# Performance work log

Measured on AMD Instinct MI355X. Metric: run time of the kernel, lower is better.

Reference implementation:

```python
import jax, jax.numpy as jnp
import numpy as np

BLOCK = 256          # block_size
K_IN = 64            # in_features // block_size
K_OUT = 64           # out_features // block_size
K_HALF = BLOCK // 2 + 1  # 129
INIT_SCALE = 0.1


def setup_inputs() -> dict:
    key = jax.random.key(0)
    kx, kr, ki = jax.random.split(key, 3)
    x = jax.random.normal(kx, (2048, K_IN * BLOCK), dtype=jnp.float32)
    W_real = jax.random.normal(kr, (K_OUT, K_IN, K_HALF), dtype=jnp.float32) * INIT_SCALE
    W_imag = jax.random.normal(ki, (K_OUT, K_IN, K_HALF), dtype=jnp.float32) * INIT_SCALE
    # match __init__: DC and Nyquist bins have zero imaginary part
    W_imag = W_imag.at[..., 0].set(0.0)
    W_imag = W_imag.at[..., -1].set(0.0)
    return {"x": x, "W_real": W_real, "W_imag": W_imag}


def _full_spectrum(W_real, W_imag):
    # Reconstruct full conjugate-symmetric spectrum per block: (k_out,k_in,BLOCK)
    H = (W_real + 1j * W_imag).astype(jnp.complex64)          # half spectrum (...,K_HALF)
    nyq = H[..., -1:].real.astype(jnp.complex64)              # real Nyquist bin (even BLOCK)
    return jnp.concatenate(
        [H[..., :-1], nyq, jnp.conj(H[..., 1:-1])[..., ::-1]], axis=-1
    )


def reference(x, W_real, W_imag):
    B = x.shape[0]
    x_blocks = x.reshape(B, K_IN, BLOCK)                      # (B, k_in, b)
    X_fft = jnp.fft.fft(x_blocks, axis=-1)                    # (B, k_in, b) complex64
    W_full = _full_spectrum(W_real, W_imag)                   # (k_out, k_in, b)
    # block-circulant matvec in frequency domain, accumulated over input blocks
    out_fft = jnp.einsum('bjf,ijf->bif', X_fft, jnp.conj(W_full))
    out = jnp.fft.ifft(out_fft, axis=-1).real                 # (B, k_out, b)
    return out.reshape(B, K_OUT * BLOCK).astype(x.dtype)
```

## Files before the change

kernel.cpp:

```cpp
#include <hip/hip_runtime.h>

#define BATCH 2048
#define KIN   64
#define KOUT  64
#define NPT   256
#define NF    129
#define FSTRIDE (BATCH * KIN)
#define XPLANE ((size_t)NF * FSTRIDE)
#define WPLANE (NF * KIN * KOUT)
#define NFP 133

#define WAVE_SYNC() __asm__ volatile("s_waitcnt lgkmcnt(0)" ::: "memory")

__device__ __forceinline__ int PHI(int i) { return i + (i >> 5); }

template<int SIGN>
__device__ __forceinline__ void fft256_r4(float2* A, float2* B, int lane) {
  float2* src = A;
  float2* dst = B;
  const float C = SIGN * (6.28318530717958647692f / 256.f);
#pragma unroll
  for (int st = 0; st < 4; ++st) {
    const int m  = 1 << (2 * st);
    const int t  = lane;
    const int jm = t & ~(m - 1);
    float2 s0 = src[PHI(t)];
    float2 s1 = src[PHI(t + 64)];
    float2 s2 = src[PHI(t + 128)];
    float2 s3 = src[PHI(t + 192)];
    float sw, cw;
    __sincosf(C * (float)jm, &sw, &cw);
    float c2 = cw * cw - sw * sw, s2w = 2.f * cw * sw;
    float c3 = c2 * cw - s2w * sw, s3w = c2 * sw + s2w * cw;
    float apcx = s0.x + s2.x, apcy = s0.y + s2.y;
    float amcx = s0.x - s2.x, amcy = s0.y - s2.y;
    float bpdx = s1.x + s3.x, bpdy = s1.y + s3.y;
    float bmdx = s1.x - s3.x, bmdy = s1.y - s3.y;
    float sbx = (SIGN < 0) ? bmdy : -bmdy;
    float sby = (SIGN < 0) ? -bmdx : bmdx;
    float t1x = amcx + sbx, t1y = amcy + sby;
    float t3x = amcx - sbx, t3y = amcy - sby;
    float t2x = apcx - bpdx, t2y = apcy - bpdy;
    const int base = t + 3 * jm;
    dst[PHI(base)]         = make_float2(apcx + bpdx, apcy + bpdy);
    dst[PHI(base + m)]     = make_float2(cw * t1x - sw * t1y, cw * t1y + sw * t1x);
    dst[PHI(base + 2 * m)] = make_float2(c2 * t2x - s2w * t2y, c2 * t2y + s2w * t2x);
    dst[PHI(base + 3 * m)] = make_float2(c3 * t3x - s3w * t3y, c3 * t3y + s3w * t3x);
    WAVE_SYNC();
    float2* tmp = src; src = dst; dst = tmp;
  }
}

__global__ __launch_bounds__(256) void k0_wtrans(const float* __restrict__ Wre,
                                                 const float* __restrict__ Wim,
                                                 float* __restrict__ Wtr,
                                                 float* __restrict__ Wti) {
  __shared__ float T[32][33];
  const int f0 = blockIdx.y * 32;
  const int d0 = blockIdx.x * 32;
  const int t  = threadIdx.x;
  const int a  = t & 31, g = t >> 5;
#pragma unroll
  for (int pl = 0; pl < 2; ++pl) {
    const float* src = pl ? Wim : Wre;
    float* dst = pl ? Wti : Wtr;
    if (pl) __syncthreads();
#pragma unroll
    for (int it = 0; it < 4; ++it) {
      int dl = g + it * 8;
      int d  = d0 + dl;
      int s  = (d & 63) * 64 + (d >> 6);
      int f  = f0 + a;
      if (f < NF) T[dl][a] = src[(size_t)s * NF + f];
    }
    __syncthreads();
#pragma unroll
    for (int it = 0; it < 4; ++it) {
      int fl = g + it * 8;
      int f  = f0 + fl;
      if (f < NF) dst[(size_t)f * (KIN * KOUT) + d0 + a] = T[a][fl];
    }
  }
}

__global__ __launch_bounds__(256) void k1_rfft(const float* __restrict__ x,
                                               float* __restrict__ Xtr,
                                               float* __restrict__ Xti) {
  __shared__ float2 fbuf[4][2][264];
  __shared__ float Sr[32 * NFP];
  __shared__ float Si[32 * NFP];
  const int wave = threadIdx.x >> 6, lane = threadIdx.x & 63;
  const int b = blockIdx.x >> 1, h = blockIdx.x & 1;
  float2* A  = fbuf[wave][0];
  float2* Bp = fbuf[wave][1];
#pragma unroll
  for (int rr = 0; rr < 8; ++rr) {
    const int jt  = rr * 4 + wave;
    const int idx = b * 64 + h * 32 + jt;
    float4 v = reinterpret_cast<const float4*>(x + (size_t)idx * NPT)[lane];
    A[PHI(4 * lane + 0)] = make_float2(v.x, 0.f);
    A[PHI(4 * lane + 1)] = make_float2(v.y, 0.f);
    A[PHI(4 * lane + 2)] = make_float2(v.z, 0.f);
    A[PHI(4 * lane + 3)] = make_float2(v.w, 0.f);
    WAVE_SYNC();
    fft256_r4<-1>(A, Bp, lane);
    float2 z0 = A[PHI(lane)];
    float2 z1 = A[PHI(lane + 64)];
    Sr[jt * NFP + lane]      = z0.x;  Si[jt * NFP + lane]      = z0.y;
    Sr[jt * NFP + lane + 64] = z1.x;  Si[jt * NFP + lane + 64] = z1.y;
    if (lane == 0) {
      float2 z2 = A[PHI(128)];
      Sr[jt * NFP + 128] = z2.x;  Si[jt * NFP + 128] = z2.y;
    }
    WAVE_SYNC();
  }
  __syncthreads();
  const int c = threadIdx.x & 31;
  const size_t baseidx = (size_t)b * 64 + h * 32 + c;
#pragma unroll
  for (int it = 0; it < 17; ++it) {
    int f = (threadIdx.x >> 5) + it * 8;
    if (f < NF) {
      Xtr[(size_t)f * FSTRIDE + baseidx] = Sr[c * NFP + f];
      Xti[(size_t)f * FSTRIDE + baseidx] = Si[c * NFP + f];
    }
  }
}

__global__ __launch_bounds__(256) void k2_cgemm(float* __restrict__ Xr,
                                                float* __restrict__ Xi,
                                                const float* __restrict__ Wtr,
                                                const float* __restrict__ Wti) {
  __shared__ __align__(16) float Xlr[64 * 68];
  __shared__ __align__(16) float Xli[64 * 68];
  __shared__ __align__(16) float Wlr[64 * 68];
  __shared__ __align__(16) float Wli[64 * 68];

  const int f  = blockIdx.y;
  const int b0 = blockIdx.x * 64;
  const int t  = threadIdx.x;
  const size_t xbase = (size_t)f * FSTRIDE + (size_t)b0 * 64;
  const float* wpr = Wtr + (size_t)f * (KIN * KOUT);
  const float* wpi = Wti + (size_t)f * (KIN * KOUT);

#pragma unroll
  for (int it = 0; it < 4; ++it) {
    int n4 = (it * 256 + t) * 4;
    int j = n4 >> 6, i0 = n4 & 63;
    float4 wr = *reinterpret_cast<const float4*>(wpr + n4);
    float4 wi = *reinterpret_cast<const float4*>(wpi + n4);
    *reinterpret_cast<float4*>(&Wlr[j * 68 + i0]) = wr;
    *reinterpret_cast<float4*>(&Wli[j * 68 + i0]) = wi;
  }
#pragma unroll
  for (int it = 0; it < 4; ++it) {
    int n4 = (it * 256 + t) * 4;
    int r = n4 >> 6, j0 = n4 & 63;
    float4 xr = *reinterpret_cast<const float4*>(Xr + xbase + n4);
    float4 xi = *reinterpret_cast<const float4*>(Xi + xbase + n4);
    Xlr[(j0 + 0) * 68 + r] = xr.x; Xlr[(j0 + 1) * 68 + r] = xr.y;
    Xlr[(j0 + 2) * 68 + r] = xr.z; Xlr[(j0 + 3) * 68 + r] = xr.w;
    Xli[(j0 + 0) * 68 + r] = xi.x; Xli[(j0 + 1) * 68 + r] = xi.y;
    Xli[(j0 + 2) * 68 + r] = xi.z; Xli[(j0 + 3) * 68 + r] = xi.w;
  }
  __syncthreads();

  const int tx = t & 15, ty = t >> 4;
  const int i0 = tx * 4, r0 = ty * 4;
  float aR[4][4] = {};
  float aI[4][4] = {};

#pragma unroll 4
  for (int j = 0; j < 64; ++j) {
    float4 xr = *reinterpret_cast<const float4*>(&Xlr[j * 68 + r0]);
    float4 xi = *reinterpret_cast<const float4*>(&Xli[j * 68 + r0]);
    float4 wr = *reinterpret_cast<const float4*>(&Wlr[j * 68 + i0]);
    float4 wi = *reinterpret_cast<const float4*>(&Wli[j * 68 + i0]);
    float xra[4] = {xr.x, xr.y, xr.z, xr.w};
    float xia[4] = {xi.x, xi.y, xi.z, xi.w};
    float wra[4] = {wr.x, wr.y, wr.z, wr.w};
    float wia[4] = {wi.x, wi.y, wi.z, wi.w};
#pragma unroll
    for (int a = 0; a < 4; ++a)
#pragma unroll
      for (int c = 0; c < 4; ++c) {
        aR[a][c] += xra[a] * wra[c] + xia[a] * wia[c];
        aI[a][c] += xia[a] * wra[c] - xra[a] * wia[c];
      }
  }

#pragma unroll
  for (int a = 0; a < 4; ++a) {
    size_t g = xbase + (size_t)(r0 + a) * 64 + i0;
    *reinterpret_cast<float4*>(&Xr[g]) = make_float4(aR[a][0], aR[a][1], aR[a][2], aR[a][3]);
    *reinterpret_cast<float4*>(&Xi[g]) = make_float4(aI[a][0], aI[a][1], aI[a][2], aI[a][3]);
  }
}

__global__ __launch_bounds__(256) void k3_irfft(const float* __restrict__ Or,
                                                const float* __restrict__ Oi,
                                                float* __restrict__ out) {
  __shared__ float2 fbuf[4][2][264];
  __shared__ float Sr[32 * NFP];
  __shared__ float Si[32 * NFP];
  const int wave = threadIdx.x >> 6, lane = threadIdx.x & 63;
  const int b = blockIdx.x >> 1, h = blockIdx.x & 1;
  const int c = threadIdx.x & 31;
  const size_t baseidx = (size_t)b * 64 + h * 32 + c;
#pragma unroll
  for (int it = 0; it < 17; ++it) {
    int f = (threadIdx.x >> 5) + it * 8;
    if (f < NF) {
      Sr[c * NFP + f] = Or[(size_t)f * FSTRIDE + baseidx];
      Si[c * NFP + f] = Oi[(size_t)f * FSTRIDE + baseidx];
    }
  }
  __syncthreads();
  float2* A  = fbuf[wave][0];
  float2* Bp = fbuf[wave][1];
#pragma unroll
  for (int rr = 0; rr < 8; ++rr) {
    const int it8 = rr * 4 + wave;
    float re0 = Sr[it8 * NFP + lane],      im0 = Si[it8 * NFP + lane];
    float re1 = Sr[it8 * NFP + lane + 64], im1 = Si[it8 * NFP + lane + 64];
    A[PHI(lane)]      = make_float2(re0, im0);
    A[PHI(lane + 64)] = make_float2(re1, im1);
    if (lane) A[PHI(256 - lane)] = make_float2(re0, -im0);
    A[PHI(192 - lane)] = make_float2(re1, -im1);
    if (lane == 0)
      A[PHI(128)] = make_float2(Sr[it8 * NFP + 128], Si[it8 * NFP + 128]);
    WAVE_SYNC();
    fft256_r4<1>(A, Bp, lane);
    const float s = 1.0f / 256.f;
    float4 o;
    o.x = A[PHI(4 * lane + 0)].x * s;
    o.y = A[PHI(4 * lane + 1)].x * s;
    o.z = A[PHI(4 * lane + 2)].x * s;
    o.w = A[PHI(4 * lane + 3)].x * s;
    const int idx = b * 64 + h * 32 + it8;
    reinterpret_cast<float4*>(out + (size_t)idx * NPT)[lane] = o;
    WAVE_SYNC();
  }
}

extern "C" void kernel_launch(void* const* d_in, const int* in_sizes, int n_in,
                              void* d_out, int out_size, void* d_ws, size_t ws_size,
                              hipStream_t stream) {
  const float* x   = (const float*)d_in[0];
  const float* Wre = (const float*)d_in[1];
  const float* Wim = (const float*)d_in[2];
  float* out = (float*)d_out;
  float* ws  = (float*)d_ws;

  float* Xr  = ws;
  float* Xi  = ws + XPLANE;
  float* Wtr = ws + 2 * XPLANE;
  float* Wti = Wtr + WPLANE;

  hipLaunchKernelGGL(k0_wtrans, dim3(128, 5), dim3(256), 0, stream,
                     Wre, Wim, Wtr, Wti);
  hipLaunchKernelGGL(k1_rfft, dim3(BATCH * 2), dim3(256), 0, stream,
                     x, Xr, Xi);
  hipLaunchKernelGGL(k2_cgemm, dim3(BATCH / 64, NF), dim3(256), 0, stream,
                     Xr, Xi, Wtr, Wti);
  hipLaunchKernelGGL(k3_irfft, dim3(BATCH * 2), dim3(256), 0, stream,
                     Xr, Xi, out);
}
```

Measured before the change: 459.0 us.

## Pack two real FFTs per complex FFT, in-place swizzled radix-4, interleaved complex workspace

Replaces the ping-pong radix-4 FFT with in-place DIF/DIT stages over an XOR-swizzled shared buffer, with twiddles computed once per thread. Two real rows are packed into one complex 256-point FFT, so the forward and inverse transforms run half as many FFTs. The intermediate spectrum is stored as interleaved float2 instead of separate real and imaginary planes. The GEMM uses a swizzled X tile, and global loads are prefetched a step ahead. This cuts FFT arithmetic, LDS traffic and memory transactions, at the cost of more index math and register pressure.

```diff
diff --git a/kernel.cpp b/kernel.cpp
--- a/kernel.cpp
+++ b/kernel.cpp
@@ -12,43 +12,69 @@
 
 #define WAVE_SYNC() __asm__ volatile("s_waitcnt lgkmcnt(0)" ::: "memory")
 
-__device__ __forceinline__ int PHI(int i) { return i + (i >> 5); }
-
-template<int SIGN>
-__device__ __forceinline__ void fft256_r4(float2* A, float2* B, int lane) {
-  float2* src = A;
-  float2* dst = B;
-  const float C = SIGN * (6.28318530717958647692f / 256.f);
-#pragma unroll
-  for (int st = 0; st < 4; ++st) {
-    const int m  = 1 << (2 * st);
-    const int t  = lane;
-    const int jm = t & ~(m - 1);
-    float2 s0 = src[PHI(t)];
-    float2 s1 = src[PHI(t + 64)];
-    float2 s2 = src[PHI(t + 128)];
-    float2 s3 = src[PHI(t + 192)];
-    float sw, cw;
-    __sincosf(C * (float)jm, &sw, &cw);
-    float c2 = cw * cw - sw * sw, s2w = 2.f * cw * sw;
-    float c3 = c2 * cw - s2w * sw, s3w = c2 * sw + s2w * cw;
-    float apcx = s0.x + s2.x, apcy = s0.y + s2.y;
-    float amcx = s0.x - s2.x, amcy = s0.y - s2.y;
-    float bpdx = s1.x + s3.x, bpdy = s1.y + s3.y;
-    float bmdx = s1.x - s3.x, bmdy = s1.y - s3.y;
-    float sbx = (SIGN < 0) ? bmdy : -bmdy;
-    float sby = (SIGN < 0) ? -bmdx : bmdx;
-    float t1x = amcx + sbx, t1y = amcy + sby;
-    float t3x = amcx - sbx, t3y = amcy - sby;
-    float t2x = apcx - bpdx, t2y = apcy - bpdy;
-    const int base = t + 3 * jm;
-    dst[PHI(base)]         = make_float2(apcx + bpdx, apcy + bpdy);
-    dst[PHI(base + m)]     = make_float2(cw * t1x - sw * t1y, cw * t1y + sw * t1x);
-    dst[PHI(base + 2 * m)] = make_float2(c2 * t2x - s2w * t2y, c2 * t2y + s2w * t2x);
-    dst[PHI(base + 3 * m)] = make_float2(c3 * t3x - s3w * t3y, c3 * t3y + s3w * t3x);
-    WAVE_SYNC();
-    float2* tmp = src; src = dst; dst = tmp;
-  }
+__device__ __forceinline__ int SWZ(int i) {
+  return i ^ (((i >> 6) & 3) << 2) ^ ((i >> 4) & 3);
+}
+__device__ __forceinline__ int REV4(int f) {
+  return ((f & 3) << 6) | ((f & 12) << 2) | ((f >> 2) & 12) | ((f >> 6) & 3);
+}
+__device__ __forceinline__ float2 cmul(float2 v, float c, float s) {
+  return make_float2(v.x * c - v.y * s, v.y * c + v.x * s);
+}
+
+struct TW { float c1, s1, c2, s2, c3, s3; };
+__device__ __forceinline__ TW mk_tw(int unit, float C) {
+  TW t; float s, c;
+  __sincosf(C * (float)unit, &s, &c);
+  t.c1 = c; t.s1 = s;
+  t.c2 = c * c - s * s;  t.s2 = 2.f * c * s;
+  t.c3 = t.c2 * c - t.s2 * s;  t.s3 = t.c2 * s + t.s2 * c;
+  return t;
+}
+
+struct Quad { int i0, i1, i2, i3; };
+__device__ __forceinline__ Quad mkquad(int base, int M) {
+  Quad q;
+  q.i0 = SWZ(base); q.i1 = SWZ(base + M);
+  q.i2 = SWZ(base + 2 * M); q.i3 = SWZ(base + 3 * M);
+  return q;
+}
+
+template<bool TWID>
+__device__ __forceinline__ void dif_stage(float2* A, const Quad& q, const TW& w) {
+  float2 a0 = A[q.i0], a1 = A[q.i1], a2 = A[q.i2], a3 = A[q.i3];
+  float t0x = a0.x + a2.x, t0y = a0.y + a2.y;
+  float t1x = a0.x - a2.x, t1y = a0.y - a2.y;
+  float t2x = a1.x + a3.x, t2y = a1.y + a3.y;
+  float t3x = a1.x - a3.x, t3y = a1.y - a3.y;
+  float2 b0 = make_float2(t0x + t2x, t0y + t2y);
+  float2 b2 = make_float2(t0x - t2x, t0y - t2y);
+  float2 b1 = make_float2(t1x + t3y, t1y - t3x);
+  float2 b3 = make_float2(t1x - t3y, t1y + t3x);
+  A[q.i0] = b0;
+  A[q.i1] = TWID ? cmul(b1, w.c1, w.s1) : b1;
+  A[q.i2] = TWID ? cmul(b2, w.c2, w.s2) : b2;
+  A[q.i3] = TWID ? cmul(b3, w.c3, w.s3) : b3;
+  WAVE_SYNC();
+}
+
+template<bool TWID>
+__device__ __forceinline__ void dit_stage(float2* A, const Quad& q, const TW& w) {
+  float2 a0 = A[q.i0], a1 = A[q.i1], a2 = A[q.i2], a3 = A[q.i3];
+  if (TWID) {
+    a1 = cmul(a1, w.c1, w.s1);
+    a2 = cmul(a2, w.c2, w.s2);
+    a3 = cmul(a3, w.c3, w.s3);
+  }
+  float Ax = a0.x + a2.x, Ay = a0.y + a2.y;
+  float Bx = a0.x - a2.x, By = a0.y - a2.y;
+  float Cx = a1.x + a3.x, Cy = a1.y + a3.y;
+  float Dx = a1.x - a3.x, Dy = a1.y - a3.y;
+  A[q.i0] = make_float2(Ax + Cx, Ay + Cy);
+  A[q.i2] = make_float2(Ax - Cx, Ay - Cy);
+  A[q.i1] = make_float2(Bx - Dy, By + Dx);
+  A[q.i3] = make_float2(Bx + Dy, By - Dx);
+  WAVE_SYNC();
 }
 
 __global__ __launch_bounds__(256) void k0_wtrans(const float* __restrict__ Wre,
@@ -84,55 +110,99 @@
 }
 
 __global__ __launch_bounds__(256) void k1_rfft(const float* __restrict__ x,
-                                               float* __restrict__ Xtr,
-                                               float* __restrict__ Xti) {
-  __shared__ float2 fbuf[4][2][264];
-  __shared__ float Sr[32 * NFP];
-  __shared__ float Si[32 * NFP];
+                                               float2* __restrict__ Xc) {
+  __shared__ float2 fbuf[4][256];
+  __shared__ float Sr[16 * NFP];
+  __shared__ float Si[16 * NFP];
   const int wave = threadIdx.x >> 6, lane = threadIdx.x & 63;
   const int b = blockIdx.x >> 1, h = blockIdx.x & 1;
-  float2* A  = fbuf[wave][0];
-  float2* Bp = fbuf[wave][1];
-#pragma unroll
-  for (int rr = 0; rr < 8; ++rr) {
-    const int jt  = rr * 4 + wave;
-    const int idx = b * 64 + h * 32 + jt;
-    float4 v = reinterpret_cast<const float4*>(x + (size_t)idx * NPT)[lane];
-    A[PHI(4 * lane + 0)] = make_float2(v.x, 0.f);
-    A[PHI(4 * lane + 1)] = make_float2(v.y, 0.f);
-    A[PHI(4 * lane + 2)] = make_float2(v.z, 0.f);
-    A[PHI(4 * lane + 3)] = make_float2(v.w, 0.f);
-    WAVE_SYNC();
-    fft256_r4<-1>(A, Bp, lane);
-    float2 z0 = A[PHI(lane)];
-    float2 z1 = A[PHI(lane + 64)];
-    Sr[jt * NFP + lane]      = z0.x;  Si[jt * NFP + lane]      = z0.y;
-    Sr[jt * NFP + lane + 64] = z1.x;  Si[jt * NFP + lane + 64] = z1.y;
-    if (lane == 0) {
-      float2 z2 = A[PHI(128)];
-      Sr[jt * NFP + 128] = z2.x;  Si[jt * NFP + 128] = z2.y;
-    }
-    WAVE_SYNC();
-  }
-  __syncthreads();
-  const int c = threadIdx.x & 31;
-  const size_t baseidx = (size_t)b * 64 + h * 32 + c;
-#pragma unroll
-  for (int it = 0; it < 17; ++it) {
-    int f = (threadIdx.x >> 5) + it * 8;
-    if (f < NF) {
-      Xtr[(size_t)f * FSTRIDE + baseidx] = Sr[c * NFP + f];
-      Xti[(size_t)f * FSTRIDE + baseidx] = Si[c * NFP + f];
-    }
-  }
-}
-
-__global__ __launch_bounds__(256) void k2_cgemm(float* __restrict__ Xr,
-                                                float* __restrict__ Xi,
+  float2* A = fbuf[wave];
+
+  const Quad q0 = mkquad(lane, 64);
+  const Quad q1 = mkquad(((lane >> 4) << 6) + (lane & 15), 16);
+  const Quad q2 = mkquad(((lane >> 2) << 4) + (lane & 3), 4);
+  const Quad q3 = mkquad(lane << 2, 1);
+  const float C = -6.28318530717958647692f / 256.f;
+  const TW tw0 = mk_tw(lane, C);
+  const TW tw1 = mk_tw(4 * (lane & 15), C);
+  const TW tw2 = mk_tw(16 * (lane & 3), C);
+  const int uf  = SWZ(REV4(lane));
+  const int ug  = SWZ(REV4(lane + 64));
+  const int ufm = SWZ(REV4((256 - lane) & 255));
+  const int ugm = SWZ(REV4(192 - lane));
+
+  const size_t rowbase = (size_t)b * 64 + h * 32;
+  float4 va = reinterpret_cast<const float4*>(x + (rowbase + 2 * wave) * NPT)[lane];
+  float4 vb = reinterpret_cast<const float4*>(x + (rowbase + 2 * wave + 1) * NPT)[lane];
+
+#pragma unroll
+  for (int half = 0; half < 2; ++half) {
+    if (half) __syncthreads();
+#pragma unroll
+    for (int uu = 0; uu < 2; ++uu) {
+      const int u = half * 2 + uu;
+      const int p = u * 4 + wave;
+      float4 na = va, nb = vb;
+      if (u < 3) {
+        const size_t nidx = rowbase + 2 * ((u + 1) * 4 + wave);
+        na = reinterpret_cast<const float4*>(x + nidx * NPT)[lane];
+        nb = reinterpret_cast<const float4*>(x + (nidx + 1) * NPT)[lane];
+      }
+      A[q3.i0] = make_float2(va.x, vb.x);
+      A[q3.i1] = make_float2(va.y, vb.y);
+      A[q3.i2] = make_float2(va.z, vb.z);
+      A[q3.i3] = make_float2(va.w, vb.w);
+      WAVE_SYNC();
+      dif_stage<true >(A, q0, tw0);
+      dif_stage<true >(A, q1, tw1);
+      dif_stage<true >(A, q2, tw2);
+      dif_stage<false>(A, q3, tw0);
+      float2 zf  = A[uf];
+      float2 zg  = A[ug];
+      float2 zfm = A[ufm];
+      float2 zgm = A[ugm];
+      const int r1 = (2 * p - half * 16) * NFP;
+      const int r2 = r1 + NFP;
+      Sr[r1 + lane]      = 0.5f * (zf.x + zfm.x);
+      Si[r1 + lane]      = 0.5f * (zf.y - zfm.y);
+      Sr[r2 + lane]      = 0.5f * (zf.y + zfm.y);
+      Si[r2 + lane]      = 0.5f * (zfm.x - zf.x);
+      Sr[r1 + lane + 64] = 0.5f * (zg.x + zgm.x);
+      Si[r1 + lane + 64] = 0.5f * (zg.y - zgm.y);
+      Sr[r2 + lane + 64] = 0.5f * (zg.y + zgm.y);
+      Si[r2 + lane + 64] = 0.5f * (zgm.x - zg.x);
+      if (lane == 0) {
+        float2 zn = A[SWZ(REV4(128))];
+        Sr[r1 + 128] = zn.x;  Si[r1 + 128] = 0.f;
+        Sr[r2 + 128] = zn.y;  Si[r2 + 128] = 0.f;
+      }
+      WAVE_SYNC();
+      va = na; vb = nb;
+    }
+    __syncthreads();
+    const int c = threadIdx.x & 15, fg = threadIdx.x >> 4;
+    const size_t baseidx = rowbase + half * 16 + c;
+#pragma unroll
+    for (int it = 0; it < 9; ++it) {
+      int f = fg + it * 16;
+      if (f < NF)
+        Xc[(size_t)f * FSTRIDE + baseidx] =
+            make_float2(Sr[c * NFP + f], Si[c * NFP + f]);
+    }
+  }
+}
+
+__device__ __forceinline__ int XIDX(int j, int r) {
+  int rc = r >> 2;
+  int rcs = (rc & 8) | ((rc ^ (j >> 1)) & 7);
+  return (j << 6) + (rcs << 2) + (r & 3);
+}
+
+__global__ __launch_bounds__(256) void k2_cgemm(float2* __restrict__ Xc,
                                                 const float* __restrict__ Wtr,
                                                 const float* __restrict__ Wti) {
-  __shared__ __align__(16) float Xlr[64 * 68];
-  __shared__ __align__(16) float Xli[64 * 68];
+  __shared__ __align__(16) float Xlr[64 * 64];
+  __shared__ __align__(16) float Xli[64 * 64];
   __shared__ __align__(16) float Wlr[64 * 68];
   __shared__ __align__(16) float Wli[64 * 68];
 
@@ -153,15 +223,13 @@
     *reinterpret_cast<float4*>(&Wli[j * 68 + i0]) = wi;
   }
 #pragma unroll
-  for (int it = 0; it < 4; ++it) {
-    int n4 = (it * 256 + t) * 4;
-    int r = n4 >> 6, j0 = n4 & 63;
-    float4 xr = *reinterpret_cast<const float4*>(Xr + xbase + n4);
-    float4 xi = *reinterpret_cast<const float4*>(Xi + xbase + n4);
-    Xlr[(j0 + 0) * 68 + r] = xr.x; Xlr[(j0 + 1) * 68 + r] = xr.y;
-    Xlr[(j0 + 2) * 68 + r] = xr.z; Xlr[(j0 + 3) * 68 + r] = xr.w;
-    Xli[(j0 + 0) * 68 + r] = xi.x; Xli[(j0 + 1) * 68 + r] = xi.y;
-    Xli[(j0 + 2) * 68 + r] = xi.z; Xli[(j0 + 3) * 68 + r] = xi.w;
+  for (int it = 0; it < 8; ++it) {
+    int n2 = (it * 256 + t) * 2;
+    int j0 = n2 & 63, r = n2 >> 6;
+    float4 v = *reinterpret_cast<const float4*>(
+                   reinterpret_cast<const float*>(Xc + xbase) + 2 * n2);
+    Xlr[XIDX(j0, r)] = v.x;      Xli[XIDX(j0, r)] = v.y;
+    Xlr[XIDX(j0 + 1, r)] = v.z;  Xli[XIDX(j0 + 1, r)] = v.w;
   }
   __syncthreads();
 
@@ -172,8 +240,8 @@
 
 #pragma unroll 4
   for (int j = 0; j < 64; ++j) {
-    float4 xr = *reinterpret_cast<const float4*>(&Xlr[j * 68 + r0]);
-    float4 xi = *reinterpret_cast<const float4*>(&Xli[j * 68 + r0]);
+    float4 xr = *reinterpret_cast<const float4*>(&Xlr[XIDX(j, r0)]);
+    float4 xi = *reinterpret_cast<const float4*>(&Xli[XIDX(j, r0)]);
     float4 wr = *reinterpret_cast<const float4*>(&Wlr[j * 68 + i0]);
     float4 wi = *reinterpret_cast<const float4*>(&Wli[j * 68 + i0]);
     float xra[4] = {xr.x, xr.y, xr.z, xr.w};
@@ -191,55 +259,96 @@
 
 #pragma unroll
   for (int a = 0; a < 4; ++a) {
-    size_t g = xbase + (size_t)(r0 + a) * 64 + i0;
-    *reinterpret_cast<float4*>(&Xr[g]) = make_float4(aR[a][0], aR[a][1], aR[a][2], aR[a][3]);
-    *reinterpret_cast<float4*>(&Xi[g]) = make_float4(aI[a][0], aI[a][1], aI[a][2], aI[a][3]);
-  }
-}
-
-__global__ __launch_bounds__(256) void k3_irfft(const float* __restrict__ Or,
-                                                const float* __restrict__ Oi,
+    float* gp = reinterpret_cast<float*>(Xc + xbase + (size_t)(r0 + a) * 64 + i0);
+    *reinterpret_cast<float4*>(gp) =
+        make_float4(aR[a][0], aI[a][0], aR[a][1], aI[a][1]);
+    *reinterpret_cast<float4*>(gp + 4) =
+        make_float4(aR[a][2], aI[a][2], aR[a][3], aI[a][3]);
+  }
+}
+
+__global__ __launch_bounds__(256) void k3_irfft(const float2* __restrict__ Oc,
                                                 float* __restrict__ out) {
-  __shared__ float2 fbuf[4][2][264];
-  __shared__ float Sr[32 * NFP];
-  __shared__ float Si[32 * NFP];
+  __shared__ float2 fbuf[4][256];
+  __shared__ float Sr[16 * NFP];
+  __shared__ float Si[16 * NFP];
   const int wave = threadIdx.x >> 6, lane = threadIdx.x & 63;
   const int b = blockIdx.x >> 1, h = blockIdx.x & 1;
-  const int c = threadIdx.x & 31;
-  const size_t baseidx = (size_t)b * 64 + h * 32 + c;
-#pragma unroll
-  for (int it = 0; it < 17; ++it) {
-    int f = (threadIdx.x >> 5) + it * 8;
-    if (f < NF) {
-      Sr[c * NFP + f] = Or[(size_t)f * FSTRIDE + baseidx];
-      Si[c * NFP + f] = Oi[(size_t)f * FSTRIDE + baseidx];
-    }
-  }
-  __syncthreads();
-  float2* A  = fbuf[wave][0];
-  float2* Bp = fbuf[wave][1];
-#pragma unroll
-  for (int rr = 0; rr < 8; ++rr) {
-    const int it8 = rr * 4 + wave;
-    float re0 = Sr[it8 * NFP + lane],      im0 = Si[it8 * NFP + lane];
-    float re1 = Sr[it8 * NFP + lane + 64], im1 = Si[it8 * NFP + lane + 64];
-    A[PHI(lane)]      = make_float2(re0, im0);
-    A[PHI(lane + 64)] = make_float2(re1, im1);
-    if (lane) A[PHI(256 - lane)] = make_float2(re0, -im0);
-    A[PHI(192 - lane)] = make_float2(re1, -im1);
-    if (lane == 0)
-      A[PHI(128)] = make_float2(Sr[it8 * NFP + 128], Si[it8 * NFP + 128]);
-    WAVE_SYNC();
-    fft256_r4<1>(A, Bp, lane);
-    const float s = 1.0f / 256.f;
-    float4 o;
-    o.x = A[PHI(4 * lane + 0)].x * s;
-    o.y = A[PHI(4 * lane + 1)].x * s;
-    o.z = A[PHI(4 * lane + 2)].x * s;
-    o.w = A[PHI(4 * lane + 3)].x * s;
-    const int idx = b * 64 + h * 32 + it8;
-    reinterpret_cast<float4*>(out + (size_t)idx * NPT)[lane] = o;
-    WAVE_SYNC();
+  float2* A = fbuf[wave];
+  const int c = threadIdx.x & 15, fg = threadIdx.x >> 4;
+  const size_t rowbase = (size_t)b * 64 + h * 32;
+
+  const Quad q0 = mkquad(lane, 64);
+  const Quad q1 = mkquad(((lane >> 4) << 6) + (lane & 15), 16);
+  const Quad q2 = mkquad(((lane >> 2) << 4) + (lane & 3), 4);
+  const Quad q3 = mkquad(lane << 2, 1);
+  const float C = 6.28318530717958647692f / 256.f;
+  const TW tw0 = mk_tw(lane, C);
+  const TW tw1 = mk_tw(4 * (lane & 15), C);
+  const TW tw2 = mk_tw(16 * (lane & 3), C);
+  const int wf  = SWZ(REV4(lane));
+  const int wg  = SWZ(REV4(lane + 64));
+  const int wfm = SWZ(REV4((256 - lane) & 255));
+  const int wgm = SWZ(REV4(192 - lane));
+
+  float2 gv[9], nv[9];
+#pragma unroll
+  for (int it = 0; it < 9; ++it) {
+    int f = fg + it * 16;
+    gv[it] = (f < NF) ? Oc[(size_t)f * FSTRIDE + rowbase + c]
+                      : make_float2(0.f, 0.f);
+  }
+#pragma unroll
+  for (int half = 0; half < 2; ++half) {
+    if (half == 0) {
+#pragma unroll
+      for (int it = 0; it < 9; ++it) {
+        int f = fg + it * 16;
+        nv[it] = (f < NF) ? Oc[(size_t)f * FSTRIDE + rowbase + 16 + c]
+                          : make_float2(0.f, 0.f);
+      }
+    }
+    if (half) __syncthreads();
+#pragma unroll
+    for (int it = 0; it < 9; ++it) {
+      int f = fg + it * 16;
+      if (f < NF) { Sr[c * NFP + f] = gv[it].x; Si[c * NFP + f] = gv[it].y; }
+    }
+    __syncthreads();
+#pragma unroll
+    for (int uu = 0; uu < 2; ++uu) {
+      const int u = half * 2 + uu;
+      const int p = u * 4 + wave;
+      const int r1 = (2 * p - half * 16) * NFP, r2 = r1 + NFP;
+      float a1r = Sr[r1 + lane],      a1i = Si[r1 + lane];
+      float b1r = Sr[r1 + lane + 64], b1i = Si[r1 + lane + 64];
+      float a2r = Sr[r2 + lane],      a2i = Si[r2 + lane];
+      float b2r = Sr[r2 + lane + 64], b2i = Si[r2 + lane + 64];
+      A[wf]  = make_float2(a1r - a2i, a1i + a2r);
+      A[wg]  = make_float2(b1r - b2i, b1i + b2r);
+      if (lane) A[wfm] = make_float2(a1r + a2i, a2r - a1i);
+      A[wgm] = make_float2(b1r + b2i, b2r - b1i);
+      if (lane == 0) {
+        float n1r = Sr[r1 + 128], n1i = Si[r1 + 128];
+        float n2r = Sr[r2 + 128], n2i = Si[r2 + 128];
+        A[SWZ(REV4(128))] = make_float2(n1r - n2i, n1i + n2r);
+      }
+      WAVE_SYNC();
+      dit_stage<false>(A, q3, tw0);
+      dit_stage<true >(A, q2, tw2);
+      dit_stage<true >(A, q1, tw1);
+      dit_stage<true >(A, q0, tw0);
+      const float s = 1.0f / 256.f;
+      float2 e0 = A[q3.i0], e1 = A[q3.i1], e2 = A[q3.i2], e3 = A[q3.i3];
+      float4 o1 = make_float4(e0.x * s, e1.x * s, e2.x * s, e3.x * s);
+      float4 o2 = make_float4(e0.y * s, e1.y * s, e2.y * s, e3.y * s);
+      const size_t idx1 = rowbase + 2 * p;
+      reinterpret_cast<float4*>(out + idx1 * NPT)[lane] = o1;
+      reinterpret_cast<float4*>(out + (idx1 + 1) * NPT)[lane] = o2;
+      WAVE_SYNC();
+    }
+#pragma unroll
+    for (int it = 0; it < 9; ++it) gv[it] = nv[it];
   }
 }
 
@@ -252,17 +361,16 @@
   float* out = (float*)d_out;
   float* ws  = (float*)d_ws;
 
-  float* Xr  = ws;
-  float* Xi  = ws + XPLANE;
+  float2* Xc = reinterpret_cast<float2*>(ws);
   float* Wtr = ws + 2 * XPLANE;
   float* Wti = Wtr + WPLANE;
 
   hipLaunchKernelGGL(k0_wtrans, dim3(128, 5), dim3(256), 0, stream,
                      Wre, Wim, Wtr, Wti);
   hipLaunchKernelGGL(k1_rfft, dim3(BATCH * 2), dim3(256), 0, stream,
-                     x, Xr, Xi);
+                     x, Xc);
   hipLaunchKernelGGL(k2_cgemm, dim3(BATCH / 64, NF), dim3(256), 0, stream,
-                     Xr, Xi, Wtr, Wti);
+                     Xc, Wtr, Wti);
   hipLaunchKernelGGL(k3_irfft, dim3(BATCH * 2), dim3(256), 0, stream,
-                     Xr, Xi, out);
-}
+                     Xc, out);
+}
```

Result: slower. 556.4 us (+21.2%).
